# Kernel optimization log

Hardware: AMD Instinct MI355X
Metric: run time of the kernel (lower is better)

Reference implementation:

```python
import jax, jax.numpy as jnp
import numpy as np

N_NODES = 2048
N_EDGES = 65536
IN_CH, HID_CH, OUT_CH = 512, 256, 128
NDIM = 5
THRESHOLD = 0.5


def _gcn(x, src, dst, ew, W, b):
    # GCNConv with self-loops (weight 1): D^{-1/2}(A+I)D^{-1/2} X W + b
    n = x.shape[0]
    deg = jnp.zeros((n,), x.dtype).at[dst].add(ew) + 1.0
    dinv = 1.0 / jnp.sqrt(deg)
    h = x @ W  # [N, out]
    coef = ew * dinv[src] * dinv[dst]  # [E]
    agg = jnp.zeros_like(h).at[dst].add(h[src] * coef[:, None])
    return agg + h / deg[:, None] + b


def _class_flags(feat, thr):
    # cosine similarity -> unnormalized Laplacian -> eigengap-based class ids
    xn = feat / (jnp.linalg.norm(feat, axis=1, keepdims=True) + 1e-8)
    S = xn @ xn.T  # [N, N]
    L = jnp.diag(jnp.sum(S, axis=1)) - S
    vals = jnp.linalg.eigvalsh(jax.lax.stop_gradient(L))  # ascending (class ids are non-diff)
    gaps = jnp.diff(vals)
    return jnp.concatenate([jnp.zeros((1,), jnp.int32),
                            jnp.cumsum((gaps > thr).astype(jnp.int32))])


def _class_avg(flags, feat):
    # per-class mean features, gathered back to each node
    n = feat.shape[0]
    sums = jax.ops.segment_sum(feat, flags, num_segments=n)
    cnts = jax.ops.segment_sum(jnp.ones((n,), feat.dtype), flags, num_segments=n)
    avg = sums / jnp.maximum(cnts, 1.0)[:, None]
    return avg[flags]


def _block(prev_gcn, skip, srcs, dsts, ews, convW, convb, linW, linb, k,
           changeW=None, changeb=None):
    gcn_out, outs = [], []
    for i in range(NDIM):
        g = _gcn(prev_gcn[i], srcs[i], dsts[i], ews[i], convW[i], convb[i])
        flags = _class_flags(g, THRESHOLD)
        lin = _class_avg(flags, g) @ linW + linb
        fir = skip[i] @ changeW + changeb if changeW is not None else skip[i]
        fea = fir + k * lin  # add_class_avg_to_node_features
        outs.append(jax.nn.relu(fir + fea))
        gcn_out.append(g)
    return gcn_out, outs


def _forward(dims, edge_indices, edge_weights, convWs, convbs, linWs, linbs,
             change1_W, change1_b, change2_W, change2_b, dimension_weights, k_save):
    srcs = [edge_indices[i, 0] for i in range(NDIM)]
    dsts = [edge_indices[i, 1] for i in range(NDIM)]
    ews = [edge_weights[i] for i in range(NDIM)]
    w = dimension_weights / jnp.sum(dimension_weights)
    g, out = _block(dims, dims, srcs, dsts, ews, convWs[0], convbs[0], linWs[0], linbs[0], k_save, change1_W, change1_b)
    g, out = _block(g, out, srcs, dsts, ews, convWs[1], convbs[1], linWs[1], linbs[1], k_save, change2_W, change2_b)
    for layer in range(2, 6):
        g, out = _block(g, out, srcs, dsts, ews, convWs[layer], convbs[layer], linWs[layer], linbs[layer], k_save)
    # dimension-weighted fusion of final per-dimension outputs
    return sum(w[i] * out[i] for i in range(NDIM))


def setup_inputs() -> dict:
    key = jax.random.key(0)
    ks = iter(jax.random.split(key, 80))
    def nrm(shape, s=0.05):
        return (jax.random.normal(next(ks), shape, jnp.float32) * s)
    inp = {}
    for i in range(NDIM):
        inp[f"dim{i+1}"] = jax.random.normal(next(ks), (N_NODES, IN_CH), jnp.float32)
    inp["edge_indices"] = jax.random.randint(next(ks), (NDIM, 2, N_EDGES), 0, N_NODES, jnp.int32)
    inp["edge_weights"] = jax.random.uniform(next(ks), (NDIM, N_EDGES), jnp.float32)
    inp["non_zero"] = N_NODES
    conv_shapes = [(IN_CH, HID_CH), (HID_CH, OUT_CH)] + [(OUT_CH, OUT_CH)] * 4
    for l, (ci, co) in enumerate(conv_shapes, start=1):
        inp[f"convW{l}"] = nrm((NDIM, ci, co))
        inp[f"convb{l}"] = nrm((NDIM, co))
    lin_shapes = [HID_CH, OUT_CH, OUT_CH, OUT_CH, OUT_CH, OUT_CH]
    names = ["preLin1", "preLin2", "preLin3", "behLin1", "behLin2", "behLin3"]
    for nm, c in zip(names, lin_shapes):
        inp[f"{nm}_W"] = nrm((c, c))
        inp[f"{nm}_b"] = nrm((c,))
    inp["change1_W"] = nrm((IN_CH, HID_CH)); inp["change1_b"] = nrm((HID_CH,))
    inp["change2_W"] = nrm((HID_CH, OUT_CH)); inp["change2_b"] = nrm((OUT_CH,))
    inp["dimension_weights"] = jnp.ones((NDIM,), jnp.float32)
    inp["k_save"] = jnp.float32(0.5)
    return inp


def reference(dim1, dim2, dim3, dim4, dim5, edge_indices, edge_weights, non_zero,
              convW1, convb1, convW2, convb2, convW3, convb3, convW4, convb4,
              convW5, convb5, convW6, convb6,
              preLin1_W, preLin1_b, preLin2_W, preLin2_b, preLin3_W, preLin3_b,
              behLin1_W, behLin1_b, behLin2_W, behLin2_b, behLin3_W, behLin3_b,
              change1_W, change1_b, change2_W, change2_b, dimension_weights, k_save):
    dims = [dim1, dim2, dim3, dim4, dim5]
    convWs = [convW1, convW2, convW3, convW4, convW5, convW6]
    convbs = [convb1, convb2, convb3, convb4, convb5, convb6]
    linWs = [preLin1_W, preLin2_W, preLin3_W, behLin1_W, behLin2_W, behLin3_W]
    linbs = [preLin1_b, preLin2_b, preLin3_b, behLin1_b, behLin2_b, behLin3_b]
    return _forward(dims, edge_indices, edge_weights, convWs, convbs, linWs, linbs,
                    change1_W, change1_b, change2_W, change2_b, dimension_weights, k_save)
```

## Files before the change

### kernel.cpp

```cpp
#include <hip/hip_runtime.h>
#include <math.h>
#include <stdint.h>

#define NN 2048
#define NE 65536
#define ND 5
#define DMX 256
#define MAXB1 2048
#define SUBD 8
#define NBF (MAXB1*SUBD+1)
#define NFMAX 1536
#define MAXRUN 1536
#define NPB 4
#define COARSE_H 1.76f
#define NUDGE 2e-3f
#define THRG 0.5f

typedef float f32x16 __attribute__((ext_vector_type(16)));
typedef float f32x8 __attribute__((ext_vector_type(8)));
typedef short s16x8 __attribute__((ext_vector_type(8)));
typedef unsigned short u16x8 __attribute__((ext_vector_type(8)));

__device__ __forceinline__ float wredSum(float v){
#pragma unroll
  for (int o=32;o>0;o>>=1) v += __shfl_down(v,o,64);
  return v;
}
__device__ __forceinline__ float wredMin(float v){
#pragma unroll
  for (int o=32;o>0;o>>=1) v = fminf(v,__shfl_down(v,o,64));
  return v;
}
__device__ __forceinline__ float wredMax(float v){
#pragma unroll
  for (int o=32;o>0;o>>=1) v = fmaxf(v,__shfl_down(v,o,64));
  return v;
}
__device__ __forceinline__ uint32_t encF(float f){
  uint32_t u = __float_as_uint(f);
  return (u & 0x80000000u) ? ~u : (u | 0x80000000u);
}
__device__ __forceinline__ float decF(uint32_t u){
  return (u & 0x80000000u) ? __uint_as_float(u ^ 0x80000000u) : __uint_as_float(~u);
}
__device__ __forceinline__ uint16_t bf16hi(float f){
  return (uint16_t)(__float_as_uint(f)>>16);
}

template<int BLK>
__device__ float bredSum(float v, float* red){
  v = wredSum(v);
  const int w = threadIdx.x >> 6;
  if ((threadIdx.x & 63) == 0) red[w] = v;
  __syncthreads();
  if (threadIdx.x == 0){
    float s = 0.f;
#pragma unroll
    for (int i=0;i<BLK/64;i++) s += red[i];
    red[0] = s;
  }
  __syncthreads();
  float r = red[0];
  __syncthreads();
  return r;
}

__global__ void k_prep(const float* __restrict__ xn, uint16_t* __restrict__ xph,
                       uint16_t* __restrict__ xpl, float* __restrict__ xpf, int co){
  const int dim = blockIdx.y;
  const int c2 = blockIdx.x;
  const int col = threadIdx.x;
  const float* x = xn + (size_t)dim*NN*co;
  const int kb = c2*8;
  u16x8 h8, l8;
  f32x8 f8;
#pragma unroll
  for (int j=0;j<8;j++){
    const float x0 = x[(size_t)(kb+j)*co + col];
    const uint16_t h = bf16hi(x0);
    h8[j] = h;
    l8[j] = bf16hi(x0 - __uint_as_float((uint32_t)h<<16));
    f8[j] = x0;
  }
  const size_t o = ((size_t)dim*(NN/8) + c2)*co + col;
  reinterpret_cast<u16x8*>(xph)[o] = h8;
  reinterpret_cast<u16x8*>(xpl)[o] = l8;
  reinterpret_cast<f32x8*>(xpf)[o] = f8;
}

template<int D, int BLK>
__device__ int evalNu(const uint16_t* __restrict__ xph, const uint16_t* __restrict__ xpl,
                      const float* __restrict__ xpf,
                      const float* __restrict__ a,
                      float t0, float dlt,
                      float* M, float* Pt, float* red, float* wrow,
                      float* scal, float* tOut)
{
  const int tid = threadIdx.x;
  float* fsc = scal + 16;

  float md = 1e30f;
  for (int i=tid;i<NN;i+=BLK) md = fminf(md, fabsf(a[i]-t0));
  md = wredMin(md);
  if ((tid & 63) == 0) red[tid>>6] = md;
  __syncthreads();
  if (tid == 0){
    float m2 = 1e30f;
    for (int i=0;i<BLK/64;i++) m2 = fminf(m2, red[i]);
    scal[1] = (m2 < 1e-3f) ? (t0 + dlt) : t0;
  }
  __syncthreads();
  const float t = scal[1];
  __syncthreads();

  float c = 0.f;
  for (int i=tid;i<NN;i+=BLK) c += (a[i] < t) ? 1.f : 0.f;
  float cnt = bredSum<BLK>(c, red);

  constexpr int BG  = D/64;
  constexpr int NBL = BG*(BG+1)/2;
  constexpr int SXT = 24;
  constexpr int NCH = NN/16;
  static_assert(BLK == NBL*64, "one wave per tile block");
  static_assert(4*D*SXT*2 <= (D*(D+1)/2)*4, "WX dbuf overlay fits in M");

  uint16_t* WX0h = reinterpret_cast<uint16_t*>(M);
  uint16_t* WX0l = WX0h + D*SXT;
  uint16_t* WX1h = WX0l + D*SXT;
  uint16_t* WX1l = WX1h + D*SXT;
  const f32x8* XPF = reinterpret_cast<const f32x8*>(xpf);

  const int wv_ = tid >> 6, lane = tid & 63;
  int bi = 0, bj = 0;
  { int rem = wv_; while (rem >= BG - bi){ rem -= BG - bi; bi++; } bj = bi + rem; }
  const int colA = bi*64 + (lane & 31);
  const int colB = bj*64 + (lane & 31);
  const int kgo  = (lane >> 5) * 8;

  f32x16 acc0, acc1, acc2, acc3;
#pragma unroll
  for (int e=0;e<16;e++){ acc0[e]=0.f; acc1[e]=0.f; acc2[e]=0.f; acc3[e]=0.f; }

  auto WCOMP = [&](int ch, int slot){
    if (tid < 16 && ch < NCH){
      float den = a[16*ch + tid] - t;
      if (fabsf(den) < 1e-5f) den = (den < 0.f) ? -1e-5f : 1e-5f;
      wrow[slot*16 + tid] = 1.0f/den;
    }
  };
  auto STAGE = [&](int ch, uint16_t* Wh, uint16_t* Wl, const float* wc){
    for (int it = tid; it < 2*D; it += BLK){
      const int kg  = it / D;
      const int col = it - kg*D;
      const f32x8 xv = XPF[(size_t)(ch*2 + kg)*D + col];
      const float4 w0 = *reinterpret_cast<const float4*>(&wc[kg*8]);
      const float4 w1 = *reinterpret_cast<const float4*>(&wc[kg*8+4]);
      const float wvv[8] = {w0.x,w0.y,w0.z,w0.w,w1.x,w1.y,w1.z,w1.w};
      u16x8 sph, spl;
#pragma unroll
      for (int j=0;j<8;j++){
        const float p0 = wvv[j]*xv[j];
        const uint16_t hp = bf16hi(p0);
        sph[j] = hp;
        spl[j] = bf16hi(p0 - __uint_as_float((uint32_t)hp<<16));
      }
      const int base = col*SXT + kg*8;
      *reinterpret_cast<u16x8*>(Wh + base) = sph;
      *reinterpret_cast<u16x8*>(Wl + base) = spl;
    }
  };
  auto MSTEP = [&](int ch, const uint16_t* Wh, const uint16_t* Wl){
    const s16x8 ah0 = *reinterpret_cast<const s16x8*>(Wh + colA*SXT + kgo);
    const s16x8 ah1 = *reinterpret_cast<const s16x8*>(Wh + (colA+32)*SXT + kgo);
    const s16x8 al0 = *reinterpret_cast<const s16x8*>(Wl + colA*SXT + kgo);
    const s16x8 al1 = *reinterpret_cast<const s16x8*>(Wl + (colA+32)*SXT + kgo);
    const size_t cgB = (size_t)(ch*2 + (lane>>5))*D;
    const s16x8 bh0 = *reinterpret_cast<const s16x8*>(xph + (cgB + colB)*8);
    const s16x8 bh1 = *reinterpret_cast<const s16x8*>(xph + (cgB + colB+32)*8);
    const s16x8 bl0 = *reinterpret_cast<const s16x8*>(xpl + (cgB + colB)*8);
    const s16x8 bl1 = *reinterpret_cast<const s16x8*>(xpl + (cgB + colB+32)*8);
    acc0 = __builtin_amdgcn_mfma_f32_32x32x16_bf16(ah0, bh0, acc0, 0,0,0);
    acc1 = __builtin_amdgcn_mfma_f32_32x32x16_bf16(ah0, bh1, acc1, 0,0,0);
    acc2 = __builtin_amdgcn_mfma_f32_32x32x16_bf16(ah1, bh0, acc2, 0,0,0);
    acc3 = __builtin_amdgcn_mfma_f32_32x32x16_bf16(ah1, bh1, acc3, 0,0,0);
    acc0 = __builtin_amdgcn_mfma_f32_32x32x16_bf16(ah0, bl0, acc0, 0,0,0);
    acc1 = __builtin_amdgcn_mfma_f32_32x32x16_bf16(ah0, bl1, acc1, 0,0,0);
    acc2 = __builtin_amdgcn_mfma_f32_32x32x16_bf16(ah1, bl0, acc2, 0,0,0);
    acc3 = __builtin_amdgcn_mfma_f32_32x32x16_bf16(ah1, bl1, acc3, 0,0,0);
    acc0 = __builtin_amdgcn_mfma_f32_32x32x16_bf16(al0, bh0, acc0, 0,0,0);
    acc1 = __builtin_amdgcn_mfma_f32_32x32x16_bf16(al0, bh1, acc1, 0,0,0);
    acc2 = __builtin_amdgcn_mfma_f32_32x32x16_bf16(al1, bh0, acc2, 0,0,0);
    acc3 = __builtin_amdgcn_mfma_f32_32x32x16_bf16(al1, bh1, acc3, 0,0,0);
  };

  WCOMP(0, 0);
  __syncthreads();
  STAGE(0, WX0h, WX0l, wrow + 0);
  WCOMP(1, 1);
  __syncthreads();
  for (int ch = 0; ch < NCH; ch += 2){
    STAGE(ch+1, WX1h, WX1l, wrow + 16);
    WCOMP(ch+2, 0);
    MSTEP(ch, WX0h, WX0l);
    __syncthreads();
    if (ch+2 < NCH) STAGE(ch+2, WX0h, WX0l, wrow + 0);
    WCOMP(ch+3, 1);
    MSTEP(ch+1, WX1h, WX1l);
    __syncthreads();
  }

  {
    const int rbase = 4*(lane>>5);
#pragma unroll
    for (int q=0;q<4;q++){
      const f32x16 A = (q==0)?acc0:((q==1)?acc1:((q==2)?acc2:acc3));
      const int ta = 2*bi + (q>>1), tb = 2*bj + (q&1);
      const int bb = tb*32 + (lane & 31);
#pragma unroll
      for (int r=0;r<16;r++){
        const int aa = ta*32 + (r&3) + 8*(r>>2) + rbase;
        if (aa <= bb)
          M[aa*D - (aa*(aa-1))/2 + (bb-aa)] = ((aa==bb)?1.f:0.f) - A[r];
      }
    }
  }

  constexpr int PS = 12;
  int neg = 0;
  for (int k0=0; k0<D; k0+=8){
    const int k1 = k0+8;
    __syncthreads();
    if (tid < 64){
      if (tid == 0){
        float B[8][8];
#pragma unroll
        for (int q=0;q<8;q++){
#pragma unroll
          for (int p=0;p<=q;p++){
            const int g = k0+p;
            B[p][q] = M[g*D - (g*(g-1))/2 + (k0+q-g)];
          }
        }
        float inv8[8];
#pragma unroll
        for (int q=0;q<8;q++){
          float d = B[q][q];
          if (d < 0.f) neg++;
          if (fabsf(d) < 1e-8f) d = (d<0.f)?-1e-8f:1e-8f;
          const float inv = 1.0f/d;
          inv8[q] = inv;
#pragma unroll
          for (int i=q+1;i<8;i++){
            const float f = B[q][i]*inv;
#pragma unroll
            for (int j=i;j<8;j++) B[i][j] = fmaf(-f, B[q][j], B[i][j]);
          }
        }
#pragma unroll
        for (int q=0;q<8;q++){
          fsc[36+q] = inv8[q];
#pragma unroll
          for (int p=0;p<=q;p++) fsc[(q*(q+1))/2 + p] = B[p][q];
        }
      }
      __asm__ __volatile__("s_waitcnt lgkmcnt(0)" ::: "memory");
      float c8[36], iv8[8];
#pragma unroll
      for (int k=0;k<36;k++) c8[k] = fsc[k];
#pragma unroll
      for (int k=0;k<8;k++) iv8[k] = fsc[36+k];
      for (int j = k1 + tid; j < D; j += 64){
        float rv[8], pt[8];
#pragma unroll
        for (int q=0;q<8;q++){
          const int g = k0+q;
          rv[q] = M[g*D - (g*(g-1))/2 + (j-g)];
        }
#pragma unroll
        for (int q=0;q<8;q++){
          float v = rv[q];
#pragma unroll
          for (int p=0;p<q;p++) v = fmaf(-c8[(q*(q+1))/2 + p], pt[p], v);
          pt[q] = v * iv8[q];
          const int g = k0+q;
          M[g*D - (g*(g-1))/2 + (j-g)] = v;
          Pt[j*PS + q] = pt[q];
        }
      }
    }
    __syncthreads();
    if (k1 < D){
      constexpr int G = BLK/4;
      const int grp = tid / G, sub = tid % G;
      for (int i0=k1; i0<D; i0+=4){
        const int i = i0 + grp;
        float cq[8];
#pragma unroll
        for (int q=0;q<8;q++){
          const int g = k0+q;
          cq[q] = M[g*D - (g*(g-1))/2 + (i-g)];
        }
        const int offi = i*D - (i*(i-1))/2;
        for (int j=i+sub; j<D; j+=G){
          const float4 p0 = *reinterpret_cast<const float4*>(&Pt[j*PS + 0]);
          const float4 p1 = *reinterpret_cast<const float4*>(&Pt[j*PS + 4]);
          float v = M[offi + (j-i)];
          v = fmaf(-cq[0],p0.x,v); v = fmaf(-cq[1],p0.y,v);
          v = fmaf(-cq[2],p0.z,v); v = fmaf(-cq[3],p0.w,v);
          v = fmaf(-cq[4],p1.x,v); v = fmaf(-cq[5],p1.y,v);
          v = fmaf(-cq[6],p1.z,v); v = fmaf(-cq[7],p1.w,v);
          M[offi + (j-i)] = v;
        }
      }
    }
  }
  if (tid == 0) ((int*)scal)[5] = neg;
  __syncthreads();
  const int negAll = ((int*)scal)[5];
  __syncthreads();

  *tOut = t;
  return negAll + (int)(cnt + 0.5f);
}

#define SMEM_D(D) (((D)*((D)+1)/2 + 12*(D) + 112)*4)

template<int D, int BLK, int WPE>
__global__ __launch_bounds__(BLK,WPE) void k_eval(const uint16_t* __restrict__ xph,
    const uint16_t* __restrict__ xpl, const float* __restrict__ xpf,
    const float* __restrict__ ab, const float* __restrict__ ctrlF,
    const int* __restrict__ ctrlI, int* __restrict__ nu1, float* __restrict__ tus1)
{
  const int dim = blockIdx.y;
  const int b = blockIdx.x;
  if (b > ctrlI[dim*8+0]) return;
  extern __shared__ float smem[];
  constexpr int TRI = D*(D+1)/2;
  float* M = smem; float* Pt = M+TRI; float* red = Pt + 12*D;
  float* wrow = red+16; float* scal = wrow+32;
  const float lo = ctrlF[dim*8+0], h1 = ctrlF[dim*8+1];
  float tU;
  int v = evalNu<D,BLK>(xph + (size_t)dim*NN*D, xpl + (size_t)dim*NN*D,
                        xpf + (size_t)dim*NN*D,
                        ab + dim*NN, lo + h1*b, NUDGE,
                        M,Pt,red,wrow,scal,&tU);
  if (threadIdx.x == 0){ nu1[dim*(MAXB1+1)+b] = v; tus1[dim*(MAXB1+1)+b] = tU; }
}

template<int D, int BLK, int WPE>
__global__ __launch_bounds__(BLK,WPE) void k_evalF(const uint16_t* __restrict__ xph,
    const uint16_t* __restrict__ xpl, const float* __restrict__ xpf,
    const float* __restrict__ ab, const float* __restrict__ ctrlF,
    const int* __restrict__ ctrlI, const int* __restrict__ fineBins,
    int* __restrict__ nuF, float* __restrict__ tusF)
{
  const int dim = blockIdx.y;
  const int task = blockIdx.x / (SUBD-1);
  int cnt = ctrlI[dim*8+3]; if (cnt > NFMAX) cnt = NFMAX;
  if (task >= cnt) return;
  const int s = blockIdx.x % (SUBD-1) + 1;
  const int bin = fineBins[dim*NFMAX + task];
  extern __shared__ float smem[];
  constexpr int TRI = D*(D+1)/2;
  float* M = smem; float* Pt = M+TRI; float* red = Pt + 12*D;
  float* wrow = red+16; float* scal = wrow+32;
  const float lo = ctrlF[dim*8+0], hf = ctrlF[dim*8+1]*(1.0f/SUBD);
  const int f = bin*SUBD + s;
  float tU;
  int v = evalNu<D,BLK>(xph + (size_t)dim*NN*D, xpl + (size_t)dim*NN*D,
                        xpf + (size_t)dim*NN*D,
                        ab + dim*NN, lo + hf*f, NUDGE,
                        M,Pt,red,wrow,scal,&tU);
  if (threadIdx.x == 0){ nuF[(size_t)dim*NBF+f] = v; tusF[(size_t)dim*NBF+f] = tU; }
}

template<int D, int BLK, int WPE>
__global__ __launch_bounds__(BLK,WPE) void k_probe(const uint16_t* __restrict__ xph,
    const uint16_t* __restrict__ xpl, const float* __restrict__ xpf,
    const float* __restrict__ ab, const int* __restrict__ ctrlI,
    const int* __restrict__ runP, const float* __restrict__ runB,
    int* __restrict__ nuP, float* __restrict__ tP)
{
  const int dim = blockIdx.y;
  const int r = blockIdx.x >> 3;
  int nr = ctrlI[dim*8+1]; if (nr > MAXRUN) nr = MAXRUN;
  if (r >= nr) return;
  const int side = (blockIdx.x >> 2) & 1;
  const int i = blockIdx.x & 3;
  extern __shared__ float smem[];
  constexpr int TRI = D*(D+1)/2;
  float* M = smem; float* Pt = M+TRI; float* red = Pt + 12*D;
  float* wrow = red+16; float* scal = wrow+32;
  const float* rb = runB + (size_t)(dim*MAXRUN + r)*4;
  const float lo = rb[side*2+0], hi = rb[side*2+1];
  const float t0 = lo + (hi - lo)*(float)(i+1)*(1.0f/(NPB+1));
  const float dlt = fminf(NUDGE, (hi-lo)*0.08f);
  float tU;
  int v = evalNu<D,BLK>(xph + (size_t)dim*NN*D, xpl + (size_t)dim*NN*D,
                        xpf + (size_t)dim*NN*D,
                        ab + dim*NN, t0, dlt,
                        M,Pt,red,wrow,scal,&tU);
  if (threadIdx.x == 0){
    const size_t o = (((size_t)dim*MAXRUN + r)*2 + side)*NPB + i;
    nuP[o] = v; tP[o] = tU;
  }
}

__global__ void k_decide(const int* __restrict__ ctrlI, const int* __restrict__ runP,
                         const float* __restrict__ runB, const int* __restrict__ nuP,
                         const float* __restrict__ tP, int* __restrict__ bnd){
  const int dim = blockIdx.x;
  int nr = ctrlI[dim*8+1]; if (nr > MAXRUN) nr = MAXRUN;
  for (int r = threadIdx.x; r < nr; r += blockDim.x){
    const int p = runP[dim*MAXRUN + r];
    const float* rb = runB + (size_t)(dim*MAXRUN + r)*4;
    float lam[2];
    for (int side=0; side<2; side++){
      const int rank = p + side;
      const size_t o = (((size_t)dim*MAXRUN + r)*2 + side)*NPB;
      float prev = rb[side*2+0];
      bool found = false; float l = 0.f;
      for (int i=0;i<NPB;i++){
        const float ti = tP[o+i];
        if (nuP[o+i] >= rank){ l = 0.5f*(prev + ti); found = true; break; }
        prev = ti;
      }
      if (!found) l = 0.5f*(prev + rb[side*2+1]);
      lam[side] = l;
    }
    if (lam[1] - lam[0] > THRG) bnd[dim*NN + p - 1] = 1;
  }
}

__global__ void k_sel(const int* __restrict__ nu1, int* ctrlI,
                      int* __restrict__ binSel, int* __restrict__ fineBins){
  const int dim = blockIdx.y;
  const int j = blockIdx.x*256 + threadIdx.x;
  const int nb1 = ctrlI[dim*8+0];
  if (j >= nb1) return;
  const int* nv = nu1 + dim*(MAXB1+1);
  if (nv[j+1] != nv[j]){
    const int slot = atomicAdd(&ctrlI[dim*8+3], 1);
    if (slot < NFMAX){ binSel[dim*MAXB1+j] = slot; fineBins[dim*NFMAX+slot] = j; }
    else binSel[dim*MAXB1+j] = -2;
  } else binSel[dim*MAXB1+j] = -1;
}

__global__ void k_fill(const int* __restrict__ nu1, const float* __restrict__ tus1,
                       const int* __restrict__ binSel, const float* __restrict__ ctrlF,
                       const int* __restrict__ ctrlI,
                       int* __restrict__ nuF, float* __restrict__ tusF){
  const int dim = blockIdx.y;
  const int f = blockIdx.x*256 + threadIdx.x;
  const int nb1 = ctrlI[dim*8+0];
  if (f > nb1*SUBD) return;
  const int j = f / SUBD, s = f % SUBD;
  const float lo = ctrlF[dim*8+0], hf = ctrlF[dim*8+1]*(1.0f/SUBD);
  int v; float tv;
  if (s == 0){ v = nu1[dim*(MAXB1+1)+j]; tv = tus1[dim*(MAXB1+1)+j]; }
  else {
    const int sel = binSel[dim*MAXB1+j];
    tv = lo + hf*f;
    if (sel == -2) v = 0x40000000 + f;
    else v = nu1[dim*(MAXB1+1)+j];
  }
  nuF[(size_t)dim*NBF+f] = v;
  tusF[(size_t)dim*NBF+f] = tv;
}

__global__ void k_runs(const int* __restrict__ nuF, const float* __restrict__ tusF,
                       int* ctrlI, int* __restrict__ runP, float* __restrict__ runB,
                       int* __restrict__ bnd){
  const int dim = blockIdx.y;
  const int b1 = blockIdx.x*256 + threadIdx.x;
  const int nbt = ctrlI[dim*8+0]*SUBD;
  if (b1 >= nbt) return;
  const int* nv = nuF + (size_t)dim*NBF;
  const float* tu = tusF + (size_t)dim*NBF;
  if (nv[b1+1] != nv[b1]) return;
  if (b1 > 0 && nv[b1-1] == nv[b1]) return;
  const int p = nv[b1];
  if (p < 1 || p > NN-1 || b1 < 1) return;
  const float tb1 = tu[b1];
  int j2 = b1;
  while (j2+1 < nbt && nv[j2+2] == nv[j2+1]){
    j2++;
    if (tu[j2+1] - tb1 > THRG){ bnd[dim*NN + p-1] = 1; return; }
  }
  if (j2 > nbt-2) return;
  const float gmin = tu[j2+1] - tb1;
  const float gmax = tu[j2+2] - tu[b1-1];
  if (gmin > THRG){ bnd[dim*NN + p-1] = 1; return; }
  if (gmax > THRG){
    const int slot = atomicAdd(&ctrlI[dim*8+1], 1);
    if (slot < MAXRUN){
      runP[dim*MAXRUN + slot] = p;
      float* rb = runB + (size_t)(dim*MAXRUN + slot)*4;
      rb[0]=tu[b1-1]; rb[1]=tu[b1]; rb[2]=tu[j2+1]; rb[3]=tu[j2+2];
    }
  }
}

__global__ void k_pw_init(float* __restrict__ vG, float* __restrict__ scACC){
  const int dim = blockIdx.x, tid = threadIdx.x;
  float* v = vG + (size_t)dim*NN;
  for (int i=tid;i<NN;i+=1024){
    uint32_t hsh = (uint32_t)i*2654435761u;
    v[i] = 1.0f + 2e-4f*(float)(hsh>>20);
  }
  if (tid == 0){ scACC[0*ND*2 + dim*2 + 0] = 1.0f; scACC[0*ND*2 + dim*2 + 1] = 0.f; }
}

template<int D>
__global__ __launch_bounds__(D) void k_pw_z(const float* __restrict__ xnb,
    const float* __restrict__ vG, float* __restrict__ zpart,
    float* __restrict__ scACC, int parReset){
  const int dim = blockIdx.y, seg = blockIdx.x, c = threadIdx.x;
  const float* x = xnb + (size_t)dim*NN*D;
  const float* v = vG + (size_t)dim*NN;
  const int i0 = seg*(NN/16);
  float acc = 0.f;
  for (int r=0;r<NN/16;r++){
    const int i = i0 + r;
    acc = fmaf(x[(size_t)i*D + c], v[i], acc);
  }
  zpart[((size_t)dim*16 + seg)*DMX + c] = acc;
  if (seg == 0 && c < 2) scACC[parReset*ND*2 + dim*2 + c] = 0.f;
}

template<int D>
__global__ __launch_bounds__(256) void k_pw_y(const float* __restrict__ xnb,
    const float* __restrict__ ab, const uint32_t* __restrict__ ctrlU,
    const float* __restrict__ zpart, float* __restrict__ vG,
    float* __restrict__ scACC, int parPrev, int parCur){
  constexpr int VEC = D/64;
  const int dim = blockIdx.y, seg = blockIdx.x, tid = threadIdx.x;
  const int w = tid >> 6, lane = tid & 63;
  const float* x = xnb + (size_t)dim*NN*D;
  const float* a = ab + dim*NN;
  float* v = vG + (size_t)dim*NN;
  __shared__ float zs[DMX];
  __shared__ float redn[4], redr[4];
  if (tid < D){
    float s = 0.f;
#pragma unroll
    for (int k=0;k<16;k++) s += zpart[((size_t)dim*16 + k)*DMX + tid];
    zs[tid] = s;
  }
  __syncthreads();
  const float amax = decF(ctrlU[dim*8+1]);
  const float invPrev = rsqrtf(fmaxf(scACC[parPrev*ND*2 + dim*2 + 0], 1e-30f));
  float zr[VEC];
#pragma unroll
  for (int k=0;k<VEC;k++) zr[k] = zs[lane*VEC + k];
  float n2 = 0.f, ray = 0.f;
  for (int r=0;r<32;r++){
    const int i = seg*(NN/16) + w*32 + r;
    const float* xr = x + (size_t)i*D + lane*VEC;
    float dot = 0.f;
#pragma unroll
    for (int k=0;k<VEC;k++) dot = fmaf(xr[k], zr[k], dot);
#pragma unroll
    for (int o=32;o>0;o>>=1) dot += __shfl_xor(dot,o,64);
    if (lane == 0){
      const float vr = v[i];
      const float y = invPrev * fmaf(amax - a[i], vr, dot);
      n2 = fmaf(y,y,n2); ray = fmaf(vr*invPrev, y, ray);
      v[i] = y;
    }
  }
  if (lane == 0){ redn[w] = n2; redr[w] = ray; }
  __syncthreads();
  if (tid == 0){
    float sn = redn[0]+redn[1]+redn[2]+redn[3];
    float sr = redr[0]+redr[1]+redr[2]+redr[3];
    atomicAdd(&scACC[parCur*ND*2 + dim*2 + 0], sn);
    atomicAdd(&scACC[parCur*ND*2 + dim*2 + 1], sr);
  }
}

__global__ void k_pw_fin(const float* __restrict__ scACC, float* __restrict__ thB,
                         int slot){
  if (threadIdx.x < ND) thB[threadIdx.x] = scACC[slot*ND*2 + threadIdx.x*2 + 1];
}

__global__ void k_init(float* deg, int* cur){
  const int dim = blockIdx.x;
  for (int i=threadIdx.x;i<NN;i+=blockDim.x){ deg[dim*NN+i] = 1.0f; cur[dim*NN+i] = 0; }
}
__global__ void k_count(const int* __restrict__ eidx, const float* __restrict__ ew,
                        float* deg, int* cur){
  const int idx = blockIdx.x*256 + threadIdx.x;
  if (idx >= ND*NE) return;
  const int dim = idx / NE, e = idx % NE;
  const int dst = eidx[(size_t)dim*2*NE + NE + e];
  atomicAdd(&cur[dim*NN + dst], 1);
  atomicAdd(&deg[dim*NN + dst], ew[(size_t)dim*NE + e]);
}
__global__ void k_prefix(int* cur, int* base){
  const int dim = blockIdx.x;
  if (threadIdx.x) return;
  int* b = base + dim*(NN+1);
  int* cc = cur + dim*NN;
  int run = 0; b[0] = 0;
  for (int i=0;i<NN;i++){ int cnt = cc[i]; cc[i] = run; b[i+1] = run + cnt; run += cnt; }
}
__global__ void k_fill_csr(const int* __restrict__ eidx, const float* __restrict__ ew,
                       const float* __restrict__ deg, int* cur, int* psrc, float* coef){
  const int idx = blockIdx.x*256 + threadIdx.x;
  if (idx >= ND*NE) return;
  const int dim = idx / NE, e = idx % NE;
  const int src = eidx[(size_t)dim*2*NE + e];
  const int dst = eidx[(size_t)dim*2*NE + NE + e];
  const int slot = atomicAdd(&cur[dim*NN + dst], 1);
  psrc[(size_t)dim*NE + slot] = src;
  const float ds = deg[dim*NN + src], dd = deg[dim*NN + dst];
  coef[(size_t)dim*NE + slot] = ew[(size_t)dim*NE + e] * (1.0f/sqrtf(ds)) * (1.0f/sqrtf(dd));
}
__global__ void k_selfw(const float* deg, float* sw){
  const int idx = blockIdx.x*256 + threadIdx.x;
  if (idx < ND*NN) sw[idx] = 1.0f/deg[idx];
}

__global__ __launch_bounds__(256) void k_gemm(const float* __restrict__ A, long long aStr,
    const float* __restrict__ W, long long wStr,
    const float* __restrict__ bias, long long bStr,
    float* __restrict__ C, long long cStr, int M, int K, int P)
{
  const int dim = blockIdx.z;
  A += (size_t)dim*aStr; W += (size_t)dim*wStr; C += (size_t)dim*cStr;
  if (bias) bias += (size_t)dim*bStr;
  __shared__ float As[64][17];
  __shared__ float Bs[16][68];
  const int tid = threadIdx.x;
  const int tx = tid % 16, ty = tid / 16;
  const int m0 = blockIdx.y*64, p0 = blockIdx.x*64;
  float acc[4][4] = {};
  for (int k0=0;k0<K;k0+=16){
    __syncthreads();
    { int r = tid/4, c4 = (tid%4)*4;
      float4 v = *reinterpret_cast<const float4*>(A + (size_t)(m0+r)*K + k0 + c4);
      As[r][c4]=v.x; As[r][c4+1]=v.y; As[r][c4+2]=v.z; As[r][c4+3]=v.w; }
    { int r = tid/16, c4 = (tid%16)*4;
      float4 v = *reinterpret_cast<const float4*>(W + (size_t)(k0+r)*P + p0 + c4);
      Bs[r][c4]=v.x; Bs[r][c4+1]=v.y; Bs[r][c4+2]=v.z; Bs[r][c4+3]=v.w; }
    __syncthreads();
#pragma unroll
    for (int kk=0;kk<16;kk++){
      float a0=As[ty*4+0][kk], a1=As[ty*4+1][kk], a2=As[ty*4+2][kk], a3=As[ty*4+3][kk];
      float b0=Bs[kk][tx*4+0], b1=Bs[kk][tx*4+1], b2=Bs[kk][tx*4+2], b3=Bs[kk][tx*4+3];
      acc[0][0]=fmaf(a0,b0,acc[0][0]); acc[0][1]=fmaf(a0,b1,acc[0][1]);
      acc[0][2]=fmaf(a0,b2,acc[0][2]); acc[0][3]=fmaf(a0,b3,acc[0][3]);
      acc[1][0]=fmaf(a1,b0,acc[1][0]); acc[1][1]=fmaf(a1,b1,acc[1][1]);
      acc[1][2]=fmaf(a1,b2,acc[1][2]); acc[1][3]=fmaf(a1,b3,acc[1][3]);
      acc[2][0]=fmaf(a2,b0,acc[2][0]); acc[2][1]=fmaf(a2,b1,acc[2][1]);
      acc[2][2]=fmaf(a2,b2,acc[2][2]); acc[2][3]=fmaf(a2,b3,acc[2][3]);
      acc[3][0]=fmaf(a3,b0,acc[3][0]); acc[3][1]=fmaf(a3,b1,acc[3][1]);
      acc[3][2]=fmaf(a3,b2,acc[3][2]); acc[3][3]=fmaf(a3,b3,acc[3][3]);
    }
  }
  for (int i=0;i<4;i++){
    for (int j=0;j<4;j++){
      const int pp = p0 + tx*4 + j;
      float v = acc[i][j];
      if (bias) v += bias[pp];
      C[(size_t)(m0+ty*4+i)*P + pp] = v;
    }
  }
}

__global__ void k_agg(const float* __restrict__ h, float* __restrict__ g,
                      const float* __restrict__ convb, const int* __restrict__ base,
                      const int* __restrict__ psrc, const float* __restrict__ coef,
                      const float* __restrict__ selfw, int co)
{
  const int i = blockIdx.x, dim = blockIdx.y, c = threadIdx.x;
  const float* hD = h + (size_t)dim*NN*co;
  const int s = base[dim*(NN+1)+i], e = base[dim*(NN+1)+i+1];
  const int* ps = psrc + (size_t)dim*NE;
  const float* cf = coef + (size_t)dim*NE;
  float acc = 0.f;
  for (int q=s;q<e;q++) acc += cf[q]*hD[(size_t)ps[q]*co + c];
  g[((size_t)dim*NN+i)*co + c] = acc + hD[(size_t)i*co + c]*selfw[dim*NN+i] + convb[dim*co + c];
}

__global__ void k_rownorm(const float* __restrict__ g, float* __restrict__ xn, int co){
  const int i = blockIdx.x, dim = blockIdx.y;
  const float* gr = g + ((size_t)dim*NN+i)*co;
  float* xr = xn + ((size_t)dim*NN+i)*co;
  float p = 0.f;
  for (int c=threadIdx.x;c<co;c+=256){ float v = gr[c]; p += v*v; }
  __shared__ float red[4];
  p = wredSum(p);
  if ((threadIdx.x&63)==0) red[threadIdx.x>>6] = p;
  __syncthreads();
  if (threadIdx.x==0) red[0] = red[0]+red[1]+red[2]+red[3];
  __syncthreads();
  const float inv = 1.0f/(sqrtf(red[0]) + 1e-8f);
  for (int c=threadIdx.x;c<co;c+=256) xr[c] = gr[c]*inv;
}

__global__ void k_colsum(const float* __restrict__ xn, float* __restrict__ sb, int co){
  const int lane = threadIdx.x & 63;
  const int seg  = threadIdx.x >> 6;
  const int c = blockIdx.x*64 + lane;
  const int dim = blockIdx.y;
  const float* x = xn + (size_t)dim*NN*co;
  float s = 0.f;
  for (int i=seg*(NN/4); i<(seg+1)*(NN/4); i++) s += x[(size_t)i*co + c];
  __shared__ float part[4][64];
  part[seg][lane] = s;
  __syncthreads();
  if (threadIdx.x < 64)
    sb[dim*DMX + c] = part[0][lane]+part[1][lane]+part[2][lane]+part[3][lane];
}

__global__ __launch_bounds__(512) void k_adot(const float* __restrict__ xn,
                       const float* __restrict__ sb,
                       float* __restrict__ ab, uint32_t* ctrlU, int co){
  const int dim = blockIdx.y;
  const int w = threadIdx.x >> 6, lane = threadIdx.x & 63;
  const int i = blockIdx.x*8 + w;
  const float* x = xn + ((size_t)dim*NN + i)*co;
  const float* s = sb + dim*DMX;
  float p = 0.f;
  for (int c=lane;c<co;c+=64) p = fmaf(x[c], s[c], p);
  p = wredSum(p);
  __shared__ uint32_t rmn[8], rmx[8];
  if (lane==0){
    ab[dim*NN+i] = p;
    const uint32_t e = encF(p);
    rmn[w] = e; rmx[w] = e;
  }
  __syncthreads();
  if (threadIdx.x==0){
    uint32_t mn = rmn[0], mx = rmx[0];
#pragma unroll
    for (int k=1;k<8;k++){
      mn = (rmn[k] < mn) ? rmn[k] : mn;
      mx = (rmx[k] > mx) ? rmx[k] : mx;
    }
    atomicMin(&ctrlU[dim*8+0], mn);
    atomicMax(&ctrlU[dim*8+1], mx);
  }
}

__global__ __launch_bounds__(256) void k_gramC(const float* __restrict__ xn,
                                               float* __restrict__ Cb, int co){
  const int dim = blockIdx.y;
  const int nbx = co/32;
  const int bx = blockIdx.x % nbx, by = blockIdx.x / nbx;
  const float* x = xn + (size_t)dim*NN*co;
  float* C = Cb + (size_t)dim*co*co;
  __shared__ float Xa[64][33];
  __shared__ float Xb[64][33];
  const int tid = threadIdx.x;
  const int ty = tid/16, tx = tid%16;
  float a00=0,a01=0,a10=0,a11=0;
  for (int i0=0;i0<NN;i0+=64){
    __syncthreads();
    for (int l=tid;l<512;l+=256){
      const int r = l/8, c4 = (l%8)*4;
      float4 va = *reinterpret_cast<const float4*>(x + (size_t)(i0+r)*co + by*32 + c4);
      Xa[r][c4]=va.x; Xa[r][c4+1]=va.y; Xa[r][c4+2]=va.z; Xa[r][c4+3]=va.w;
      float4 vb = *reinterpret_cast<const float4*>(x + (size_t)(i0+r)*co + bx*32 + c4);
      Xb[r][c4]=vb.x; Xb[r][c4+1]=vb.y; Xb[r][c4+2]=vb.z; Xb[r][c4+3]=vb.w;
    }
    __syncthreads();
#pragma unroll 8
    for (int r=0;r<64;r++){
      const float u0=Xa[r][ty*2], u1=Xa[r][ty*2+1], w0=Xb[r][tx*2], w1=Xb[r][tx*2+1];
      a00=fmaf(u0,w0,a00); a01=fmaf(u0,w1,a01); a10=fmaf(u1,w0,a10); a11=fmaf(u1,w1,a11);
    }
  }
  const int ca = by*32 + ty*2, cb = bx*32 + tx*2;
  C[(size_t)(ca+0)*co + cb+0]=a00; C[(size_t)(ca+0)*co + cb+1]=a01;
  C[(size_t)(ca+1)*co + cb+0]=a10; C[(size_t)(ca+1)*co + cb+1]=a11;
}

__global__ void k_layerinit(int* bnd, uint32_t* ctrlU, int* ctrlI){
  const int dim = blockIdx.x;
  for (int i=threadIdx.x;i<NN;i+=blockDim.x) bnd[dim*NN+i] = 0;
  if (threadIdx.x==0){
    ctrlU[dim*8+0] = 0xFFFFFFFFu;
    ctrlU[dim*8+1] = 0u;
    ctrlI[dim*8+1] = 0;
    ctrlI[dim*8+3] = 0;
  }
}

__global__ __launch_bounds__(256) void k_bounds(const float* __restrict__ Cb,
                         const uint32_t* ctrlU, const float* __restrict__ thB,
                         float* ctrlF, int* ctrlI, int co){
  const int dim = blockIdx.x, tid = threadIdx.x;
  const float* C = Cb + (size_t)dim*co*co;
  __shared__ float red[4];
  float rs = 0.f;
  if (tid < co){
    const float* row = C + (size_t)tid*co;
    for (int b=0;b<co;b++) rs += fabsf(row[b]);
  }
  float mx = wredMax(rs);
  if ((tid&63)==0) red[tid>>6] = mx;
  __syncthreads();
  if (tid==0){
    const float gersh = fmaxf(fmaxf(red[0],red[1]), fmaxf(red[2],red[3]));
    const float amin = decF(ctrlU[dim*8+0]);
    const float amax = decF(ctrlU[dim*8+1]);
    const float th = thB[dim];
    const float loG = amin - gersh;
    const float loP = amax - th - (0.02f*fabsf(th) + 0.5f);
    const float lo = fmaxf(loG, loP) - 0.05f;
    const float hi = amax + 0.1f;
    int nb = (int)ceilf((hi - lo)/COARSE_H);
    if (nb > MAXB1) nb = MAXB1;
    if (nb < 8) nb = 8;
    ctrlF[dim*8+0] = lo;
    ctrlF[dim*8+1] = (hi - lo)/nb;
    ctrlI[dim*8+0] = nb;
  }
}

__global__ void k_flags(const int* __restrict__ bnd, int* flags, int* cstart, int* ctrlI){
  const int dim = blockIdx.x;
  if (threadIdx.x) return;
  const int* b = bnd + dim*NN;
  int* f = flags + dim*NN;
  int* cs = cstart + dim*(NN+1);
  int cur = 0; f[0] = 0; cs[0] = 0;
  for (int i=1;i<NN;i++){
    cur += b[i-1];
    f[i] = cur;
    if (b[i-1]) cs[cur] = i;
  }
  ctrlI[dim*8+2] = cur+1;
  cs[cur+1] = NN;
}

__global__ void k_cavg(const float* __restrict__ g, const int* __restrict__ cstart,
                       const int* __restrict__ ctrlI, float* __restrict__ cavg, int co){
  const int dim = blockIdx.y;
  const int nc = ctrlI[dim*8+2];
  const float* gD = g + (size_t)dim*NN*co;
  const int cc = threadIdx.x;
  for (int c = blockIdx.x; c < nc; c += gridDim.x){
    const int s = cstart[dim*(NN+1)+c], e = cstart[dim*(NN+1)+c+1];
    const float inv = 1.0f/(float)(e - s);
    if (cc < co){
      float acc = 0.f;
      for (int i=s;i<e;i++) acc += gD[(size_t)i*co + cc];
      cavg[((size_t)dim*NN + c)*co + cc] = acc*inv;
    }
  }
}

__global__ void k_clin(const float* __restrict__ cavg, const float* __restrict__ linW,
                       const float* __restrict__ linb, float* __restrict__ clin,
                       const int* __restrict__ ctrlI, int co){
  const int dim = blockIdx.y;
  const int nc = ctrlI[dim*8+2];
  __shared__ float row[DMX];
  const int tid = threadIdx.x;
  for (int c = blockIdx.x; c < nc; c += gridDim.x){
    const float* av = cavg + ((size_t)dim*NN + c)*co;
    __syncthreads();
    if (tid < co) row[tid] = av[tid];
    __syncthreads();
    if (tid < co){
      float s = linb[tid];
      for (int k=0;k<co;k++) s = fmaf(row[k], linW[(size_t)k*co + tid], s);
      clin[((size_t)dim*NN + c)*co + tid] = s;
    }
  }
}

__global__ void k_out(const float* __restrict__ fir, const float* __restrict__ clin,
                      const int* __restrict__ flags, const float* __restrict__ ksv,
                      float* __restrict__ out, int co){
  const int i = blockIdx.x, dim = blockIdx.y, c = threadIdx.x;
  const float kv = ksv[0];
  const int cls = flags[dim*NN+i];
  const float fv = fir[((size_t)dim*NN+i)*co + c];
  const float lv = clin[((size_t)dim*NN+cls)*co + c];
  const float o = 2.f*fv + kv*lv;
  out[((size_t)dim*NN+i)*co + c] = (o > 0.f) ? o : 0.f;
}

__global__ void k_final(const float* __restrict__ outL, const float* __restrict__ dimw,
                        float* __restrict__ o){
  const int i = blockIdx.x, c = threadIdx.x;
  float w[ND]; float ws = 0.f;
#pragma unroll
  for (int d=0;d<ND;d++){ w[d] = dimw[d]; ws += w[d]; }
  float v = 0.f;
#pragma unroll
  for (int d=0;d<ND;d++) v += (w[d]/ws) * outL[((size_t)d*NN + i)*128 + c];
  o[(size_t)i*128 + c] = v;
}

extern "C" void kernel_launch(void* const* d_in, const int* in_sizes, int n_in,
                              void* d_out, int out_size, void* d_ws, size_t ws_size,
                              hipStream_t stream)
{
  const float* dims_in[ND];
  for (int d=0;d<ND;d++) dims_in[d] = (const float*)d_in[d];
  const int*   eidx = (const int*)d_in[5];
  const float* ew   = (const float*)d_in[6];
  const float* convW[6]; const float* convb[6];
  for (int l=0;l<6;l++){ convW[l] = (const float*)d_in[8+2*l]; convb[l] = (const float*)d_in[9+2*l]; }
  const float* linW[6]; const float* linb[6];
  for (int l=0;l<6;l++){ linW[l] = (const float*)d_in[20+2*l]; linb[l] = (const float*)d_in[21+2*l]; }
  const float* ch1W = (const float*)d_in[32]; const float* ch1b = (const float*)d_in[33];
  const float* ch2W = (const float*)d_in[34]; const float* ch2b = (const float*)d_in[35];
  const float* dimw = (const float*)d_in[36]; const float* ksv = (const float*)d_in[37];

  char* p = (char*)d_ws;
  auto take = [&](size_t bytes)->char*{
    char* r = p; p += (bytes + 255) & ~(size_t)255; return r;
  };
  int*   csr_base = (int*)  take((size_t)ND*(NN+1)*4);
  int*   csr_cur  = (int*)  take((size_t)ND*NN*4);
  int*   csr_psrc = (int*)  take((size_t)ND*NE*4);
  float* csr_coef = (float*)take((size_t)ND*NE*4);
  float* deg      = (float*)take((size_t)ND*NN*4);
  float* selfw    = (float*)take((size_t)ND*NN*4);
  float* gA   = (float*)take((size_t)ND*NN*DMX*4);
  float* gB   = (float*)take((size_t)ND*NN*DMX*4);
  float* outA = (float*)take((size_t)ND*NN*DMX*4);
  float* outB = (float*)take((size_t)ND*NN*DMX*4);
  float* hbuf = (float*)take((size_t)ND*NN*DMX*4);
  float* xnbuf= (float*)take((size_t)ND*NN*DMX*4);
  float* cavg = (float*)take((size_t)ND*NN*DMX*4);
  uint16_t* xph = (uint16_t*)take((size_t)ND*NN*DMX*2);
  uint16_t* xpl = (uint16_t*)take((size_t)ND*NN*DMX*2);
  float* xpf  = (float*)take((size_t)ND*NN*DMX*4);
  float* abuf = (float*)take((size_t)ND*NN*4);
  float* sbuf = (float*)take((size_t)ND*DMX*4);
  float* Cbuf = (float*)take((size_t)ND*DMX*DMX*4);
  float* vpow = (float*)take((size_t)ND*NN*4);
  float* zpartG=(float*)take((size_t)ND*16*DMX*4);
  float* scACC =(float*)take((size_t)2*ND*2*4);
  int*   nu1  = (int*)  take((size_t)ND*(MAXB1+1)*4);
  float* tus1 = (float*)take((size_t)ND*(MAXB1+1)*4);
  int*   nuF  = (int*)  take((size_t)ND*NBF*4);
  float* tusF = (float*)take((size_t)ND*NBF*4);
  int*   binSel=(int*)  take((size_t)ND*MAXB1*4);
  int*   fineBins=(int*)take((size_t)ND*NFMAX*4);
  int*   runP = (int*)  take((size_t)ND*MAXRUN*4);
  float* runB = (float*)take((size_t)ND*MAXRUN*4*4);
  int*   nuP  = (int*)  take((size_t)ND*MAXRUN*2*NPB*4);
  float* tP   = (float*)take((size_t)ND*MAXRUN*2*NPB*4);
  int*   bnd  = (int*)  take((size_t)ND*NN*4);
  int*   flagsA=(int*)  take((size_t)ND*NN*4);
  int*   cstart=(int*)  take((size_t)ND*(NN+1)*4);
  float* ctrlF= (float*)take((size_t)ND*8*4);
  uint32_t* ctrlU = (uint32_t*)take((size_t)ND*8*4);
  int*   ctrlI= (int*)  take((size_t)ND*8*4);
  float* thB  = (float*)take((size_t)ND*4);
  (void)ws_size; (void)in_sizes; (void)n_in; (void)out_size;

  {
    void (*pe)(const uint16_t*,const uint16_t*,const float*,const float*,const float*,const int*,int*,float*) = k_eval<256,640,1>;
    hipFuncSetAttribute((const void*)pe, hipFuncAttributeMaxDynamicSharedMemorySize, SMEM_D(256));
    void (*pf)(const uint16_t*,const uint16_t*,const float*,const float*,const float*,const int*,const int*,int*,float*) = k_evalF<256,640,1>;
    hipFuncSetAttribute((const void*)pf, hipFuncAttributeMaxDynamicSharedMemorySize, SMEM_D(256));
    void (*pp)(const uint16_t*,const uint16_t*,const float*,const float*,const int*,const int*,const float*,int*,float*) = k_probe<256,640,1>;
    hipFuncSetAttribute((const void*)pp, hipFuncAttributeMaxDynamicSharedMemorySize, SMEM_D(256));
  }

  k_init<<<ND, 256, 0, stream>>>(deg, csr_cur);
  k_count<<<(ND*NE+255)/256, 256, 0, stream>>>(eidx, ew, deg, csr_cur);
  k_prefix<<<ND, 64, 0, stream>>>(csr_cur, csr_base);
  k_fill_csr<<<(ND*NE+255)/256, 256, 0, stream>>>(eidx, ew, deg, csr_cur, csr_psrc, csr_coef);
  k_selfw<<<(ND*NN+255)/256, 256, 0, stream>>>(deg, selfw);

  float* gbufs[2] = {gA, gB};
  float* obufs[2] = {outA, outB};
  const float* gPrev = nullptr;
  const float* oPrev = nullptr;

  for (int l=0;l<6;l++){
    const int co = (l==0) ? 256 : 128;
    const int ci = (l==0) ? 512 : ((l==1) ? 256 : 128);
    float* gCur = gbufs[l&1];
    float* oCur = obufs[l&1];

    if (l==0){
      for (int d=0;d<ND;d++)
        k_gemm<<<dim3(256/64, NN/64, 1), 256, 0, stream>>>(
          dims_in[d], 0, convW[0] + (size_t)d*512*256, 0, nullptr, 0,
          hbuf + (size_t)d*NN*256, 0, NN, 512, 256);
    } else {
      k_gemm<<<dim3(co/64, NN/64, ND), 256, 0, stream>>>(
        gPrev, (long long)NN*ci, convW[l], (long long)ci*co, nullptr, 0,
        hbuf, (long long)NN*co, NN, ci, co);
    }

    k_layerinit<<<ND, 256, 0, stream>>>(bnd, ctrlU, ctrlI);
    k_agg<<<dim3(NN, ND), co, 0, stream>>>(hbuf, gCur, convb[l], csr_base, csr_psrc,
                                           csr_coef, selfw, co);
    k_rownorm<<<dim3(NN, ND), 256, 0, stream>>>(gCur, xnbuf, co);
    k_prep<<<dim3(NN/8, ND), co, 0, stream>>>(xnbuf, xph, xpl, xpf, co);
    k_colsum<<<dim3(co/64, ND), 256, 0, stream>>>(xnbuf, sbuf, co);
    k_adot<<<dim3(NN/8, ND), 512, 0, stream>>>(xnbuf, sbuf, abuf, ctrlU, co);
    k_gramC<<<dim3((co/32)*(co/32), ND), 256, 0, stream>>>(xnbuf, Cbuf, co);

    k_pw_init<<<ND, 1024, 0, stream>>>(vpow, scACC);
    if (l==0){
      for (int it=0; it<33; it++){
        const int sp = it & 1, sc = sp ^ 1;
        k_pw_z<256><<<dim3(16, ND), 256, 0, stream>>>(xnbuf, vpow, zpartG, scACC, sc);
        k_pw_y<256><<<dim3(16, ND), 256, 0, stream>>>(xnbuf, abuf, ctrlU, zpartG, vpow, scACC, sp, sc);
      }
    } else {
      for (int it=0; it<33; it++){
        const int sp = it & 1, sc = sp ^ 1;
        k_pw_z<128><<<dim3(16, ND), 128, 0, stream>>>(xnbuf, vpow, zpartG, scACC, sc);
        k_pw_y<128><<<dim3(16, ND), 256, 0, stream>>>(xnbuf, abuf, ctrlU, zpartG, vpow, scACC, sp, sc);
      }
    }
    k_pw_fin<<<1, 64, 0, stream>>>(scACC, thB, 1);

    k_bounds<<<ND, 256, 0, stream>>>(Cbuf, ctrlU, thB, ctrlF, ctrlI, co);

    if (l==0){
      k_eval<256,640,1><<<dim3(MAXB1+1, ND), 640, SMEM_D(256), stream>>>(xph, xpl, xpf, abuf, ctrlF, ctrlI, nu1, tus1);
      k_sel<<<dim3((MAXB1+255)/256, ND), 256, 0, stream>>>(nu1, ctrlI, binSel, fineBins);
      k_fill<<<dim3((NBF+255)/256, ND), 256, 0, stream>>>(nu1, tus1, binSel, ctrlF, ctrlI, nuF, tusF);
      k_evalF<256,640,1><<<dim3(NFMAX*(SUBD-1), ND), 640, SMEM_D(256), stream>>>(xph, xpl, xpf, abuf, ctrlF, ctrlI, fineBins, nuF, tusF);
      k_runs<<<dim3((NBF+255)/256, ND), 256, 0, stream>>>(nuF, tusF, ctrlI, runP, runB, bnd);
      k_probe<256,640,1><<<dim3(MAXRUN*2*NPB, ND), 640, SMEM_D(256), stream>>>(xph, xpl, xpf, abuf, ctrlI, runP, runB, nuP, tP);
      k_decide<<<ND, 256, 0, stream>>>(ctrlI, runP, runB, nuP, tP, bnd);
    } else {
      k_eval<128,192,4><<<dim3(MAXB1+1, ND), 192, SMEM_D(128), stream>>>(xph, xpl, xpf, abuf, ctrlF, ctrlI, nu1, tus1);
      k_sel<<<dim3((MAXB1+255)/256, ND), 256, 0, stream>>>(nu1, ctrlI, binSel, fineBins);
      k_fill<<<dim3((NBF+255)/256, ND), 256, 0, stream>>>(nu1, tus1, binSel, ctrlF, ctrlI, nuF, tusF);
      k_evalF<128,192,4><<<dim3(NFMAX*(SUBD-1), ND), 192, SMEM_D(128), stream>>>(xph, xpl, xpf, abuf, ctrlF, ctrlI, fineBins, nuF, tusF);
      k_runs<<<dim3((NBF+255)/256, ND), 256, 0, stream>>>(nuF, tusF, ctrlI, runP, runB, bnd);
      k_probe<128,192,4><<<dim3(MAXRUN*2*NPB, ND), 192, SMEM_D(128), stream>>>(xph, xpl, xpf, abuf, ctrlI, runP, runB, nuP, tP);
      k_decide<<<ND, 256, 0, stream>>>(ctrlI, runP, runB, nuP, tP, bnd);
    }

    k_flags<<<ND, 64, 0, stream>>>(bnd, flagsA, cstart, ctrlI);
    k_cavg<<<dim3(128, ND), 256, 0, stream>>>(gCur, cstart, ctrlI, cavg, co);
    k_clin<<<dim3(128, ND), 256, 0, stream>>>(cavg, linW[l], linb[l], xnbuf, ctrlI, co);

    const float* firPtr;
    if (l==0){
      for (int d=0;d<ND;d++)
        k_gemm<<<dim3(256/64, NN/64, 1), 256, 0, stream>>>(
          dims_in[d], 0, ch1W, 0, ch1b, 0, hbuf + (size_t)d*NN*256, 0, NN, 512, 256);
      firPtr = hbuf;
    } else if (l==1){
      k_gemm<<<dim3(128/64, NN/64, ND), 256, 0, stream>>>(
        oPrev, (long long)NN*256, ch2W, 0, ch2b, 0, hbuf, (long long)NN*128, NN, 256, 128);
      firPtr = hbuf;
    } else {
      firPtr = oPrev;
    }

    k_out<<<dim3(NN, ND), co, 0, stream>>>(firPtr, xnbuf, flagsA, ksv, oCur, co);

    gPrev = gCur; oPrev = oCur;
  }

  k_final<<<NN, 128, 0, stream>>>(oPrev, dimw, (float*)d_out);
}
```

Baseline: 33.18 ms.

## Fuse power-iteration launches into one cooperative kernel with grid syncs

Replaces the 67-plus small kernel launches per layer (init, 33 z/y pairs, finalize) with a single cooperative kernel that loops 33 iterations and uses grid.sync between phases. This targets launch overhead and inter-kernel gaps in the power iteration, which runs on only 80 blocks. In exchange it relies on cooperative launch support and grid-wide barriers, and the z phase now runs inside 256-thread blocks where only D threads do work.

```diff
diff --git a/kernel.cpp b/kernel.cpp
--- a/kernel.cpp
+++ b/kernel.cpp
@@ -1,6 +1,9 @@
 #include <hip/hip_runtime.h>
+#include <hip/hip_cooperative_groups.h>
 #include <math.h>
 #include <stdint.h>
+
+namespace cg = cooperative_groups;
 
 #define NN 2048
 #define NE 65536
@@ -501,39 +504,14 @@
   }
 }
 
-__global__ void k_pw_init(float* __restrict__ vG, float* __restrict__ scACC){
-  const int dim = blockIdx.x, tid = threadIdx.x;
-  float* v = vG + (size_t)dim*NN;
-  for (int i=tid;i<NN;i+=1024){
-    uint32_t hsh = (uint32_t)i*2654435761u;
-    v[i] = 1.0f + 2e-4f*(float)(hsh>>20);
-  }
-  if (tid == 0){ scACC[0*ND*2 + dim*2 + 0] = 1.0f; scACC[0*ND*2 + dim*2 + 1] = 0.f; }
-}
-
 template<int D>
-__global__ __launch_bounds__(D) void k_pw_z(const float* __restrict__ xnb,
-    const float* __restrict__ vG, float* __restrict__ zpart,
-    float* __restrict__ scACC, int parReset){
-  const int dim = blockIdx.y, seg = blockIdx.x, c = threadIdx.x;
-  const float* x = xnb + (size_t)dim*NN*D;
-  const float* v = vG + (size_t)dim*NN;
-  const int i0 = seg*(NN/16);
-  float acc = 0.f;
-  for (int r=0;r<NN/16;r++){
-    const int i = i0 + r;
-    acc = fmaf(x[(size_t)i*D + c], v[i], acc);
-  }
-  zpart[((size_t)dim*16 + seg)*DMX + c] = acc;
-  if (seg == 0 && c < 2) scACC[parReset*ND*2 + dim*2 + c] = 0.f;
-}
-
-template<int D>
-__global__ __launch_bounds__(256) void k_pw_y(const float* __restrict__ xnb,
+__global__ __launch_bounds__(256) void k_pw_coop(const float* __restrict__ xnb,
     const float* __restrict__ ab, const uint32_t* __restrict__ ctrlU,
-    const float* __restrict__ zpart, float* __restrict__ vG,
-    float* __restrict__ scACC, int parPrev, int parCur){
+    float* __restrict__ vG, float* __restrict__ zpart,
+    float* __restrict__ scACC, float* __restrict__ thB)
+{
   constexpr int VEC = D/64;
+  cg::grid_group grid = cg::this_grid();
   const int dim = blockIdx.y, seg = blockIdx.x, tid = threadIdx.x;
   const int w = tid >> 6, lane = tid & 63;
   const float* x = xnb + (size_t)dim*NN*D;
@@ -541,47 +519,71 @@
   float* v = vG + (size_t)dim*NN;
   __shared__ float zs[DMX];
   __shared__ float redn[4], redr[4];
-  if (tid < D){
-    float s = 0.f;
-#pragma unroll
-    for (int k=0;k<16;k++) s += zpart[((size_t)dim*16 + k)*DMX + tid];
-    zs[tid] = s;
-  }
-  __syncthreads();
-  const float amax = decF(ctrlU[dim*8+1]);
-  const float invPrev = rsqrtf(fmaxf(scACC[parPrev*ND*2 + dim*2 + 0], 1e-30f));
-  float zr[VEC];
-#pragma unroll
-  for (int k=0;k<VEC;k++) zr[k] = zs[lane*VEC + k];
-  float n2 = 0.f, ray = 0.f;
-  for (int r=0;r<32;r++){
-    const int i = seg*(NN/16) + w*32 + r;
-    const float* xr = x + (size_t)i*D + lane*VEC;
-    float dot = 0.f;
-#pragma unroll
-    for (int k=0;k<VEC;k++) dot = fmaf(xr[k], zr[k], dot);
-#pragma unroll
-    for (int o=32;o>0;o>>=1) dot += __shfl_xor(dot,o,64);
-    if (lane == 0){
-      const float vr = v[i];
-      const float y = invPrev * fmaf(amax - a[i], vr, dot);
-      n2 = fmaf(y,y,n2); ray = fmaf(vr*invPrev, y, ray);
-      v[i] = y;
-    }
-  }
-  if (lane == 0){ redn[w] = n2; redr[w] = ray; }
-  __syncthreads();
-  if (tid == 0){
-    float sn = redn[0]+redn[1]+redn[2]+redn[3];
-    float sr = redr[0]+redr[1]+redr[2]+redr[3];
-    atomicAdd(&scACC[parCur*ND*2 + dim*2 + 0], sn);
-    atomicAdd(&scACC[parCur*ND*2 + dim*2 + 1], sr);
-  }
-}
-
-__global__ void k_pw_fin(const float* __restrict__ scACC, float* __restrict__ thB,
-                         int slot){
-  if (threadIdx.x < ND) thB[threadIdx.x] = scACC[slot*ND*2 + threadIdx.x*2 + 1];
+
+  {
+    const int i = seg*(NN/16) + tid;
+    if (tid < NN/16){
+      uint32_t hsh = (uint32_t)i*2654435761u;
+      v[i] = 1.0f + 2e-4f*(float)(hsh>>20);
+    }
+    if (seg == 0 && tid == 0){
+      scACC[0*ND*2 + dim*2 + 0] = 1.0f;
+      scACC[0*ND*2 + dim*2 + 1] = 0.f;
+    }
+  }
+  grid.sync();
+
+  for (int it=0; it<33; it++){
+    const int sp = it & 1, sc = sp ^ 1;
+    if (tid < D){
+      float acc = 0.f;
+      const int i0 = seg*(NN/16);
+      for (int r=0;r<NN/16;r++)
+        acc = fmaf(x[(size_t)(i0+r)*D + tid], v[i0+r], acc);
+      zpart[((size_t)dim*16 + seg)*DMX + tid] = acc;
+    }
+    if (seg == 0 && tid < 2) scACC[sc*ND*2 + dim*2 + tid] = 0.f;
+    grid.sync();
+    if (tid < D){
+      float s = 0.f;
+#pragma unroll
+      for (int k=0;k<16;k++) s += zpart[((size_t)dim*16 + k)*DMX + tid];
+      zs[tid] = s;
+    }
+    __syncthreads();
+    const float amax = decF(ctrlU[dim*8+1]);
+    const float invPrev = rsqrtf(fmaxf(scACC[sp*ND*2 + dim*2 + 0], 1e-30f));
+    float zr[VEC];
+#pragma unroll
+    for (int k=0;k<VEC;k++) zr[k] = zs[lane*VEC + k];
+    float n2 = 0.f, ray = 0.f;
+    for (int r=0;r<32;r++){
+      const int i = seg*(NN/16) + w*32 + r;
+      const float* xr = x + (size_t)i*D + lane*VEC;
+      float dot = 0.f;
+#pragma unroll
+      for (int k=0;k<VEC;k++) dot = fmaf(xr[k], zr[k], dot);
+#pragma unroll
+      for (int o=32;o>0;o>>=1) dot += __shfl_xor(dot,o,64);
+      if (lane == 0){
+        const float vr = v[i];
+        const float y = invPrev * fmaf(amax - a[i], vr, dot);
+        n2 = fmaf(y,y,n2); ray = fmaf(vr*invPrev, y, ray);
+        v[i] = y;
+      }
+    }
+    if (lane == 0){ redn[w] = n2; redr[w] = ray; }
+    __syncthreads();
+    if (tid == 0){
+      float sn = redn[0]+redn[1]+redn[2]+redn[3];
+      float sr = redr[0]+redr[1]+redr[2]+redr[3];
+      atomicAdd(&scACC[sc*ND*2 + dim*2 + 0], sn);
+      atomicAdd(&scACC[sc*ND*2 + dim*2 + 1], sr);
+    }
+    __syncthreads();
+    grid.sync();
+  }
+  if (seg == 0 && tid == 0) thB[dim] = scACC[1*ND*2 + dim*2 + 1];
 }
 
 __global__ void k_init(float* deg, int* cur){
@@ -1005,21 +1007,19 @@
     k_adot<<<dim3(NN/8, ND), 512, 0, stream>>>(xnbuf, sbuf, abuf, ctrlU, co);
     k_gramC<<<dim3((co/32)*(co/32), ND), 256, 0, stream>>>(xnbuf, Cbuf, co);
 
-    k_pw_init<<<ND, 1024, 0, stream>>>(vpow, scACC);
-    if (l==0){
-      for (int it=0; it<33; it++){
-        const int sp = it & 1, sc = sp ^ 1;
-        k_pw_z<256><<<dim3(16, ND), 256, 0, stream>>>(xnbuf, vpow, zpartG, scACC, sc);
-        k_pw_y<256><<<dim3(16, ND), 256, 0, stream>>>(xnbuf, abuf, ctrlU, zpartG, vpow, scACC, sp, sc);
+    {
+      void* pwArgs[] = { (void*)&xnbuf, (void*)&abuf, (void*)&ctrlU,
+                         (void*)&vpow, (void*)&zpartG, (void*)&scACC, (void*)&thB };
+      if (l==0){
+        void (*f256)(const float*,const float*,const uint32_t*,float*,float*,float*,float*) = k_pw_coop<256>;
+        hipLaunchCooperativeKernel((const void*)f256, dim3(16,ND), dim3(256),
+                                   pwArgs, 0, stream);
+      } else {
+        void (*f128)(const float*,const float*,const uint32_t*,float*,float*,float*,float*) = k_pw_coop<128>;
+        hipLaunchCooperativeKernel((const void*)f128, dim3(16,ND), dim3(256),
+                                   pwArgs, 0, stream);
       }
-    } else {
-      for (int it=0; it<33; it++){
-        const int sp = it & 1, sc = sp ^ 1;
-        k_pw_z<128><<<dim3(16, ND), 128, 0, stream>>>(xnbuf, vpow, zpartG, scACC, sc);
-        k_pw_y<128><<<dim3(16, ND), 256, 0, stream>>>(xnbuf, abuf, ctrlU, zpartG, vpow, scACC, sp, sc);
-      }
-    }
-    k_pw_fin<<<1, 64, 0, stream>>>(scACC, thB, 1);
+    }
 
     k_bounds<<<ND, 256, 0, stream>>>(Cbuf, ctrlU, thB, ctrlF, ctrlI, co);
 
```

Result: slower. 36.91 ms (+11.2%).
